# Kernel optimization log

Measured on AMD Instinct MI355X. Metric: run time of the kernel, lower is better.

## Reference

```python
import jax, jax.numpy as jnp
import numpy as np

NUM_HEADS = 8
GS = 7  # group_size (window) side

def _relative_position_index():
    # static index table, matches the torch meshgrid('ij') construction
    coords = np.stack(np.meshgrid(np.arange(GS), np.arange(GS), indexing='ij'))  # (2,GS,GS)
    cf = coords.reshape(2, -1)                                 # (2, 49)
    rel = cf[:, :, None] - cf[:, None, :]                      # (2, 49, 49)
    rel = rel.transpose(1, 2, 0).copy()                        # (49, 49, 2)
    rel[..., 0] += GS - 1
    rel[..., 1] += GS - 1
    rel[..., 0] *= 2 * GS - 1
    return rel.sum(-1)                                         # (49, 49) in [0, 169)

REL_INDEX = jnp.asarray(_relative_position_index())

def setup_inputs() -> dict:
    key = jax.random.key(0)
    ks = jax.random.split(key, 5)
    B, N, C = 2048, 49, 256
    HID = 64
    return {
        'q': jax.random.normal(ks[0], (B, N, C), dtype=jnp.float32),
        'k': jax.random.normal(ks[1], (B, N, C), dtype=jnp.float32),
        'v': jax.random.normal(ks[2], (B, N, C), dtype=jnp.float32),
        'W1': jax.random.normal(ks[3], (2, HID), dtype=jnp.float32) * 0.1,
        'b1': jnp.zeros((HID,), dtype=jnp.float32),
        'W2': jax.random.normal(ks[4], (HID, NUM_HEADS), dtype=jnp.float32) * 0.1,
        'b2': jnp.zeros((NUM_HEADS,), dtype=jnp.float32),
        'H': 56,
        'W': 56,
    }

def _bias_table(W1, b1, W2, b2):
    # biases: (2*GS-1)^2 relative offsets, dpb_pos modeled as 2-layer MLP 2->HID->heads
    r = jnp.arange(1 - GS, GS, dtype=jnp.float32)
    bh, bw = jnp.meshgrid(r, r, indexing='ij')
    biases = jnp.stack([bh.ravel(), bw.ravel()], axis=1)       # (169, 2)
    pos = jax.nn.relu(biases @ W1 + b1) @ W2 + b2              # (169, heads)
    return pos[REL_INDEX].transpose(2, 0, 1)                   # (heads, 49, 49)

def reference(q, k, v, W1, b1, W2, b2, H, W):
    B, N, C = q.shape
    h = NUM_HEADS
    d = C // h
    scale = d ** -0.5
    qh = q.reshape(B, N, h, d)
    kh = k.reshape(B, N, h, d)
    vh = v.reshape(B, N, h, d)
    attn = jnp.einsum('bihd,bjhd->bhij', qh, kh) * scale       # (B,h,N,N)
    bias = _bias_table(W1, b1, W2, b2)                         # (h,49,49)
    if H == 7 and W == 7:
        attn = attn.at[:, :, 0:GS * GS, 0:GS * GS].add(bias[None])
    else:
        attn = attn + bias[None]
    attn = jax.nn.softmax(attn, axis=-1)
    out = jnp.einsum('bhij,bjhd->bihd', attn, vh).reshape(B, N, C)
    return out
```

## Files before the change

### kernel.cpp

```cpp
#include <hip/hip_runtime.h>

typedef __attribute__((ext_vector_type(4))) _Float16 f16x4;
typedef __attribute__((ext_vector_type(8))) _Float16 f16x8;
typedef __attribute__((ext_vector_type(4))) float f32x4;

#define NWIN 49
#define NH 8
#define CCH 256

__device__ __forceinline__ uint cvt2_u32(float a, float b) {
    auto t = __builtin_amdgcn_cvt_pkrtz(a, b);
    return *(uint*)&t;
}
__device__ __forceinline__ f16x4 mk4(uint a, uint b) {
    union { uint u[2]; f16x4 v; } x;
    x.u[0] = a; x.u[1] = b;
    return x.v;
}
__device__ __forceinline__ f16x8 mk8(uint a, uint b, uint c, uint d) {
    union { uint u[4]; f16x8 v; } x;
    x.u[0] = a; x.u[1] = b; x.u[2] = c; x.u[3] = d;
    return x.v;
}

__global__ void pos_mlp_kernel(const float* __restrict__ W1, const float* __restrict__ b1,
                               const float* __restrict__ W2, const float* __restrict__ b2,
                               float* __restrict__ pos) {
    int idx = blockIdx.x * blockDim.x + threadIdx.x;
    if (idx >= 169) return;
    float bh = (float)(idx / 13) - 6.0f;
    float bw = (float)(idx % 13) - 6.0f;
    float outv[NH];
#pragma unroll
    for (int t = 0; t < NH; ++t) outv[t] = b2[t];
    for (int u = 0; u < 64; ++u) {
        float hv = fmaf(bh, W1[u], fmaf(bw, W1[64 + u], b1[u]));
        hv = fmaxf(hv, 0.0f);
#pragma unroll
        for (int t = 0; t < NH; ++t) outv[t] = fmaf(hv, W2[u * NH + t], outv[t]);
    }
#pragma unroll
    for (int t = 0; t < NH; ++t) pos[idx * NH + t] = outv[t];
}

__global__ void bias_frag_kernel(const float* __restrict__ pos, float* __restrict__ bfrag) {
    int blk = blockIdx.x;
    int it = blk & 3, jt = (blk >> 2) & 3, h = blk >> 4;
    int lane = threadIdx.x;
    int g = lane >> 4, l15 = lane & 15;
    int i = it * 16 + l15;
    float4 v;
    float* vp = (float*)&v;
#pragma unroll
    for (int r = 0; r < 4; ++r) {
        int j = jt * 16 + g * 4 + r;
        float val;
        if (j >= NWIN) val = -1e30f;
        else if (i >= NWIN) val = 0.0f;
        else {
            int rel = (i / 7 - j / 7 + 6) * 13 + (i % 7 - j % 7 + 6);
            val = pos[rel * NH + h] * 1.4426950408889634f;
        }
        vp[r] = val;
    }
    *(float4*)(bfrag + (size_t)blk * 256 + lane * 4) = v;
}

__global__ __launch_bounds__(512, 3) void attn_kernel(
    const float* __restrict__ q, const float* __restrict__ k,
    const float* __restrict__ v, const float* __restrict__ bfrag,
    float* __restrict__ out) {
    const int nper = (int)(gridDim.x >> 3);
    const int b = ((int)blockIdx.x & 7) * nper + ((int)blockIdx.x >> 3);

    const int tid = threadIdx.x;
    const int w = tid >> 6, lane = tid & 63;
    const int h = w;
    const int g = lane >> 4, l15 = lane & 15;
    const size_t base = (size_t)b * (NWIN * CCH) + h * 32;

    float4 kraw[4][2], qraw[4][2];
#pragma unroll
    for (int t = 0; t < 4; ++t) {
        int row = t * 16 + l15;
        int rc = row < NWIN ? row : NWIN - 1;
        const float* kp = k + base + (size_t)rc * CCH + g * 8;
        const float* qp = q + base + (size_t)rc * CCH + g * 8;
        kraw[t][0] = *(const float4*)kp; kraw[t][1] = *(const float4*)(kp + 4);
        qraw[t][0] = *(const float4*)qp; qraw[t][1] = *(const float4*)(qp + 4);
    }
    float vv[4][2][4];
#pragma unroll
    for (int jt = 0; jt < 4; ++jt)
#pragma unroll
        for (int nt = 0; nt < 2; ++nt)
#pragma unroll
            for (int r = 0; r < 4; ++r) {
                int j = jt * 16 + 4 * g + r;
                int jc = j < NWIN ? j : NWIN - 1;
                vv[jt][nt][r] = v[base + (size_t)jc * CCH + nt * 16 + l15];
            }

#pragma unroll
    for (int t = 0; t < 4; ++t)
        asm volatile("" :: "v"(kraw[t][0].x), "v"(kraw[t][1].x),
                           "v"(qraw[t][0].x), "v"(qraw[t][1].x));

    f16x8 ka16[4], qb16[4];
#pragma unroll
    for (int t = 0; t < 4; ++t) {
        float4 a = kraw[t][0], c = kraw[t][1];
        ka16[t] = mk8(cvt2_u32(a.x, a.y), cvt2_u32(a.z, a.w),
                      cvt2_u32(c.x, c.y), cvt2_u32(c.z, c.w));
        float4 d = qraw[t][0], e = qraw[t][1];
        qb16[t] = mk8(cvt2_u32(d.x, d.y), cvt2_u32(d.z, d.w),
                      cvt2_u32(e.x, e.y), cvt2_u32(e.z, e.w));
    }

    f32x4 acc[4][4];
#pragma unroll
    for (int jt = 0; jt < 4; ++jt)
#pragma unroll
        for (int it = 0; it < 4; ++it) {
            f32x4 a = {0.f, 0.f, 0.f, 0.f};
            acc[jt][it] = __builtin_amdgcn_mfma_f32_16x16x32_f16(ka16[jt], qb16[it], a, 0, 0, 0);
        }

    f32x4 bb[4][4];
#pragma unroll
    for (int jt = 0; jt < 4; ++jt)
#pragma unroll
        for (int it = 0; it < 4; ++it)
            bb[jt][it] = *(const f32x4*)(bfrag + (size_t)((h * 4 + jt) * 4 + it) * 256 + lane * 4);

    const float scale2 = 0.17677669529663687f * 1.4426950408889634f;
    f16x4 pfrag[4][4];
#pragma unroll
    for (int it = 0; it < 4; ++it) {
        float p[16];
        float s = 0.0f;
#pragma unroll
        for (int jt = 0; jt < 4; ++jt)
#pragma unroll
            for (int r = 0; r < 4; ++r) {
                float e = __builtin_amdgcn_exp2f(fmaf(acc[jt][it][r], scale2, bb[jt][it][r]));
                p[jt * 4 + r] = e;
                s += e;
            }
        s += __shfl_xor(s, 16);
        s += __shfl_xor(s, 32);
        const float inv = 1.0f / s;
#pragma unroll
        for (int jt = 0; jt < 4; ++jt)
            pfrag[jt][it] = mk4(cvt2_u32(p[jt * 4 + 0] * inv, p[jt * 4 + 1] * inv),
                                cvt2_u32(p[jt * 4 + 2] * inv, p[jt * 4 + 3] * inv));
    }

#pragma unroll
    for (int jt = 0; jt < 4; ++jt)
        asm volatile("" :: "v"(vv[jt][0][0]), "v"(vv[jt][0][3]),
                           "v"(vv[jt][1][0]), "v"(vv[jt][1][3]));
    f16x4 vfrag[4][2];
#pragma unroll
    for (int jt = 0; jt < 4; ++jt)
#pragma unroll
        for (int nt = 0; nt < 2; ++nt)
            vfrag[jt][nt] = mk4(cvt2_u32(vv[jt][nt][0], vv[jt][nt][1]),
                                cvt2_u32(vv[jt][nt][2], vv[jt][nt][3]));

    f32x4 oacc[4][2];
#pragma unroll
    for (int mt = 0; mt < 4; ++mt)
#pragma unroll
        for (int nt = 0; nt < 2; ++nt) oacc[mt][nt] = (f32x4){0.f, 0.f, 0.f, 0.f};
#pragma unroll
    for (int jt = 0; jt < 4; ++jt)
#pragma unroll
        for (int mt = 0; mt < 4; ++mt)
#pragma unroll
            for (int nt = 0; nt < 2; ++nt)
                oacc[mt][nt] = __builtin_amdgcn_mfma_f32_16x16x16f16(pfrag[jt][mt], vfrag[jt][nt],
                                                                     oacc[mt][nt], 0, 0, 0);

#pragma unroll
    for (int mt = 0; mt < 4; ++mt)
#pragma unroll
        for (int r = 0; r < 4; ++r) {
            int i = mt * 16 + g * 4 + r;
            if (i < NWIN) {
                float* op = out + base + (size_t)i * CCH + l15;
                op[0]  = oacc[mt][0][r];
                op[16] = oacc[mt][1][r];
            }
        }
}

extern "C" void kernel_launch(void* const* d_in, const int* in_sizes, int n_in,
                              void* d_out, int out_size, void* d_ws, size_t ws_size,
                              hipStream_t stream) {
    const float* q  = (const float*)d_in[0];
    const float* k  = (const float*)d_in[1];
    const float* v  = (const float*)d_in[2];
    const float* W1 = (const float*)d_in[3];
    const float* b1 = (const float*)d_in[4];
    const float* W2 = (const float*)d_in[5];
    const float* b2 = (const float*)d_in[6];

    float* pos   = (float*)d_ws;
    float* bfrag = (float*)((char*)d_ws + 8192);
    float* out   = (float*)d_out;

    const int B = in_sizes[0] / (NWIN * CCH);

    pos_mlp_kernel<<<1, 192, 0, stream>>>(W1, b1, W2, b2, pos);
    bias_frag_kernel<<<128, 64, 0, stream>>>(pos, bfrag);
    attn_kernel<<<B, 512, 0, stream>>>(q, k, v, bfrag, out);
}
```

Baseline: 108.6 us.

## Process two windows per block, fuse bias MLP kernels, store bias in fp16

Each attention block now handles two batch windows. It preloads Q/K for both up front and issues window B's V loads before computing window B, so memory latency overlaps with compute and bias fragments are loaded once per two windows. The two bias setup kernels are merged into one that evaluates the MLP per fragment element and packs the bias as fp16, which removes a launch and halves bias reads. In exchange register pressure rises (launch bounds drop to 2 blocks/SM), the grid is halved, and fp16 bias adds some rounding. The kernel also assumes B is even.

```diff
diff --git a/kernel.cpp b/kernel.cpp
--- a/kernel.cpp
+++ b/kernel.cpp
@@ -22,74 +22,82 @@
     x.u[0] = a; x.u[1] = b; x.u[2] = c; x.u[3] = d;
     return x.v;
 }
-
-__global__ void pos_mlp_kernel(const float* __restrict__ W1, const float* __restrict__ b1,
-                               const float* __restrict__ W2, const float* __restrict__ b2,
-                               float* __restrict__ pos) {
-    int idx = blockIdx.x * blockDim.x + threadIdx.x;
-    if (idx >= 169) return;
-    float bh = (float)(idx / 13) - 6.0f;
-    float bw = (float)(idx % 13) - 6.0f;
-    float outv[NH];
-#pragma unroll
-    for (int t = 0; t < NH; ++t) outv[t] = b2[t];
-    for (int u = 0; u < 64; ++u) {
-        float hv = fmaf(bh, W1[u], fmaf(bw, W1[64 + u], b1[u]));
-        hv = fmaxf(hv, 0.0f);
-#pragma unroll
-        for (int t = 0; t < NH; ++t) outv[t] = fmaf(hv, W2[u * NH + t], outv[t]);
-    }
-#pragma unroll
-    for (int t = 0; t < NH; ++t) pos[idx * NH + t] = outv[t];
-}
-
-__global__ void bias_frag_kernel(const float* __restrict__ pos, float* __restrict__ bfrag) {
+__device__ __forceinline__ float bias_elem(uint2 bb, int r) {
+    union { uint u; _Float16 h[2]; } x;
+    x.u = (r < 2) ? bb.x : bb.y;
+    return (float)x.h[r & 1];
+}
+
+__global__ void bias16_kernel(const float* __restrict__ W1, const float* __restrict__ b1,
+                              const float* __restrict__ W2, const float* __restrict__ b2,
+                              uint* __restrict__ bfrag16) {
     int blk = blockIdx.x;
     int it = blk & 3, jt = (blk >> 2) & 3, h = blk >> 4;
     int lane = threadIdx.x;
     int g = lane >> 4, l15 = lane & 15;
     int i = it * 16 + l15;
-    float4 v;
-    float* vp = (float*)&v;
+    int ic = i < NWIN ? i : NWIN - 1;
+    float dh[4], dw[4], outv[4];
+#pragma unroll
+    for (int r = 0; r < 4; ++r) {
+        int j = jt * 16 + g * 4 + r;
+        int jc = j < NWIN ? j : NWIN - 1;
+        dh[r] = (float)(ic / 7 - jc / 7);
+        dw[r] = (float)(ic % 7 - jc % 7);
+        outv[r] = b2[h];
+    }
+    for (int u = 0; u < 64; ++u) {
+        float w1a = W1[u], w1b = W1[64 + u], bu = b1[u], w2 = W2[u * NH + h];
+#pragma unroll
+        for (int r = 0; r < 4; ++r) {
+            float hv = fmaxf(fmaf(dh[r], w1a, fmaf(dw[r], w1b, bu)), 0.0f);
+            outv[r] = fmaf(hv, w2, outv[r]);
+        }
+    }
+    _Float16 hv16[4];
 #pragma unroll
     for (int r = 0; r < 4; ++r) {
         int j = jt * 16 + g * 4 + r;
         float val;
-        if (j >= NWIN) val = -1e30f;
+        if (j >= NWIN) val = -__builtin_inff();
         else if (i >= NWIN) val = 0.0f;
-        else {
-            int rel = (i / 7 - j / 7 + 6) * 13 + (i % 7 - j % 7 + 6);
-            val = pos[rel * NH + h] * 1.4426950408889634f;
-        }
-        vp[r] = val;
-    }
-    *(float4*)(bfrag + (size_t)blk * 256 + lane * 4) = v;
-}
-
-__global__ __launch_bounds__(512, 3) void attn_kernel(
+        else val = outv[r] * 1.4426950408889634f;
+        hv16[r] = (_Float16)val;
+    }
+    union { _Float16 h[4]; uint2 u; } pk;
+    pk.h[0] = hv16[0]; pk.h[1] = hv16[1]; pk.h[2] = hv16[2]; pk.h[3] = hv16[3];
+    *(uint2*)(bfrag16 + (size_t)blk * 128 + lane * 2) = pk.u;
+}
+
+__global__ __launch_bounds__(512, 2) void attn_kernel(
     const float* __restrict__ q, const float* __restrict__ k,
-    const float* __restrict__ v, const float* __restrict__ bfrag,
+    const float* __restrict__ v, const uint* __restrict__ bfrag16,
     float* __restrict__ out) {
     const int nper = (int)(gridDim.x >> 3);
-    const int b = ((int)blockIdx.x & 7) * nper + ((int)blockIdx.x >> 3);
+    const int bw = ((int)blockIdx.x & 7) * nper + ((int)blockIdx.x >> 3);
 
     const int tid = threadIdx.x;
     const int w = tid >> 6, lane = tid & 63;
     const int h = w;
     const int g = lane >> 4, l15 = lane & 15;
-    const size_t base = (size_t)b * (NWIN * CCH) + h * 32;
-
-    float4 kraw[4][2], qraw[4][2];
+    const size_t baseA = (size_t)(2 * bw) * (NWIN * CCH) + h * 32;
+    const size_t baseB = baseA + (size_t)NWIN * CCH;
+
+    float4 kA[4][2], qA[4][2], kB[4][2], qB[4][2];
 #pragma unroll
     for (int t = 0; t < 4; ++t) {
         int row = t * 16 + l15;
         int rc = row < NWIN ? row : NWIN - 1;
-        const float* kp = k + base + (size_t)rc * CCH + g * 8;
-        const float* qp = q + base + (size_t)rc * CCH + g * 8;
-        kraw[t][0] = *(const float4*)kp; kraw[t][1] = *(const float4*)(kp + 4);
-        qraw[t][0] = *(const float4*)qp; qraw[t][1] = *(const float4*)(qp + 4);
-    }
-    float vv[4][2][4];
+        const float* kpA = k + baseA + (size_t)rc * CCH + g * 8;
+        const float* qpA = q + baseA + (size_t)rc * CCH + g * 8;
+        const float* kpB = k + baseB + (size_t)rc * CCH + g * 8;
+        const float* qpB = q + baseB + (size_t)rc * CCH + g * 8;
+        kA[t][0] = *(const float4*)kpA; kA[t][1] = *(const float4*)(kpA + 4);
+        qA[t][0] = *(const float4*)qpA; qA[t][1] = *(const float4*)(qpA + 4);
+        kB[t][0] = *(const float4*)kpB; kB[t][1] = *(const float4*)(kpB + 4);
+        qB[t][0] = *(const float4*)qpB; qB[t][1] = *(const float4*)(qpB + 4);
+    }
+    float vA[4][2][4];
 #pragma unroll
     for (int jt = 0; jt < 4; ++jt)
 #pragma unroll
@@ -98,25 +106,27 @@
             for (int r = 0; r < 4; ++r) {
                 int j = jt * 16 + 4 * g + r;
                 int jc = j < NWIN ? j : NWIN - 1;
-                vv[jt][nt][r] = v[base + (size_t)jc * CCH + nt * 16 + l15];
-            }
+                vA[jt][nt][r] = v[baseA + (size_t)jc * CCH + nt * 16 + l15];
+            }
+    uint2 bb16[4][4];
+#pragma unroll
+    for (int jt = 0; jt < 4; ++jt)
+#pragma unroll
+        for (int it = 0; it < 4; ++it)
+            bb16[jt][it] = *(const uint2*)(bfrag16 + (size_t)((h * 4 + jt) * 4 + it) * 128 + lane * 2);
+
+    const float scale2 = 0.17677669529663687f * 1.4426950408889634f;
 
 #pragma unroll
     for (int t = 0; t < 4; ++t)
-        asm volatile("" :: "v"(kraw[t][0].x), "v"(kraw[t][1].x),
-                           "v"(qraw[t][0].x), "v"(qraw[t][1].x));
-
+        asm volatile("" :: "v"(kA[t][0].x), "v"(kA[t][1].x), "v"(qA[t][0].x), "v"(qA[t][1].x));
     f16x8 ka16[4], qb16[4];
 #pragma unroll
     for (int t = 0; t < 4; ++t) {
-        float4 a = kraw[t][0], c = kraw[t][1];
-        ka16[t] = mk8(cvt2_u32(a.x, a.y), cvt2_u32(a.z, a.w),
-                      cvt2_u32(c.x, c.y), cvt2_u32(c.z, c.w));
-        float4 d = qraw[t][0], e = qraw[t][1];
-        qb16[t] = mk8(cvt2_u32(d.x, d.y), cvt2_u32(d.z, d.w),
-                      cvt2_u32(e.x, e.y), cvt2_u32(e.z, e.w));
-    }
-
+        float4 a = kA[t][0], c = kA[t][1], d = qA[t][0], e = qA[t][1];
+        ka16[t] = mk8(cvt2_u32(a.x, a.y), cvt2_u32(a.z, a.w), cvt2_u32(c.x, c.y), cvt2_u32(c.z, c.w));
+        qb16[t] = mk8(cvt2_u32(d.x, d.y), cvt2_u32(d.z, d.w), cvt2_u32(e.x, e.y), cvt2_u32(e.z, e.w));
+    }
     f32x4 acc[4][4];
 #pragma unroll
     for (int jt = 0; jt < 4; ++jt)
@@ -125,16 +135,11 @@
             f32x4 a = {0.f, 0.f, 0.f, 0.f};
             acc[jt][it] = __builtin_amdgcn_mfma_f32_16x16x32_f16(ka16[jt], qb16[it], a, 0, 0, 0);
         }
-
-    f32x4 bb[4][4];
-#pragma unroll
-    for (int jt = 0; jt < 4; ++jt)
-#pragma unroll
-        for (int it = 0; it < 4; ++it)
-            bb[jt][it] = *(const f32x4*)(bfrag + (size_t)((h * 4 + jt) * 4 + it) * 256 + lane * 4);
-
-    const float scale2 = 0.17677669529663687f * 1.4426950408889634f;
-    f16x4 pfrag[4][4];
+#pragma unroll
+    for (int jt = 0; jt < 4; ++jt)
+        asm volatile("" :: "v"(bb16[jt][0].x), "v"(bb16[jt][1].x), "v"(bb16[jt][2].x), "v"(bb16[jt][3].x));
+
+    f16x4 pf[4][4];
 #pragma unroll
     for (int it = 0; it < 4; ++it) {
         float p[16];
@@ -143,7 +148,7 @@
         for (int jt = 0; jt < 4; ++jt)
 #pragma unroll
             for (int r = 0; r < 4; ++r) {
-                float e = __builtin_amdgcn_exp2f(fmaf(acc[jt][it][r], scale2, bb[jt][it][r]));
+                float e = __builtin_amdgcn_exp2f(fmaf(acc[jt][it][r], scale2, bias_elem(bb16[jt][it], r)));
                 p[jt * 4 + r] = e;
                 s += e;
             }
@@ -152,22 +157,18 @@
         const float inv = 1.0f / s;
 #pragma unroll
         for (int jt = 0; jt < 4; ++jt)
-            pfrag[jt][it] = mk4(cvt2_u32(p[jt * 4 + 0] * inv, p[jt * 4 + 1] * inv),
-                                cvt2_u32(p[jt * 4 + 2] * inv, p[jt * 4 + 3] * inv));
-    }
-
-#pragma unroll
-    for (int jt = 0; jt < 4; ++jt)
-        asm volatile("" :: "v"(vv[jt][0][0]), "v"(vv[jt][0][3]),
-                           "v"(vv[jt][1][0]), "v"(vv[jt][1][3]));
-    f16x4 vfrag[4][2];
-#pragma unroll
-    for (int jt = 0; jt < 4; ++jt)
-#pragma unroll
-        for (int nt = 0; nt < 2; ++nt)
-            vfrag[jt][nt] = mk4(cvt2_u32(vv[jt][nt][0], vv[jt][nt][1]),
-                                cvt2_u32(vv[jt][nt][2], vv[jt][nt][3]));
-
+            pf[jt][it] = mk4(cvt2_u32(p[jt * 4 + 0] * inv, p[jt * 4 + 1] * inv),
+                             cvt2_u32(p[jt * 4 + 2] * inv, p[jt * 4 + 3] * inv));
+    }
+#pragma unroll
+    for (int jt = 0; jt < 4; ++jt)
+        asm volatile("" :: "v"(vA[jt][0][0]), "v"(vA[jt][0][3]), "v"(vA[jt][1][0]), "v"(vA[jt][1][3]));
+    f16x4 vf[4][2];
+#pragma unroll
+    for (int jt = 0; jt < 4; ++jt)
+#pragma unroll
+        for (int nt = 0; nt < 2; ++nt)
+            vf[jt][nt] = mk4(cvt2_u32(vA[jt][nt][0], vA[jt][nt][1]), cvt2_u32(vA[jt][nt][2], vA[jt][nt][3]));
     f32x4 oacc[4][2];
 #pragma unroll
     for (int mt = 0; mt < 4; ++mt)
@@ -179,16 +180,93 @@
         for (int mt = 0; mt < 4; ++mt)
 #pragma unroll
             for (int nt = 0; nt < 2; ++nt)
-                oacc[mt][nt] = __builtin_amdgcn_mfma_f32_16x16x16f16(pfrag[jt][mt], vfrag[jt][nt],
-                                                                     oacc[mt][nt], 0, 0, 0);
-
+                oacc[mt][nt] = __builtin_amdgcn_mfma_f32_16x16x16f16(pf[jt][mt], vf[jt][nt], oacc[mt][nt], 0, 0, 0);
 #pragma unroll
     for (int mt = 0; mt < 4; ++mt)
 #pragma unroll
         for (int r = 0; r < 4; ++r) {
             int i = mt * 16 + g * 4 + r;
             if (i < NWIN) {
-                float* op = out + base + (size_t)i * CCH + l15;
+                float* op = out + baseA + (size_t)i * CCH + l15;
+                op[0]  = oacc[mt][0][r];
+                op[16] = oacc[mt][1][r];
+            }
+        }
+
+    float vB[4][2][4];
+#pragma unroll
+    for (int jt = 0; jt < 4; ++jt)
+#pragma unroll
+        for (int nt = 0; nt < 2; ++nt)
+#pragma unroll
+            for (int r = 0; r < 4; ++r) {
+                int j = jt * 16 + 4 * g + r;
+                int jc = j < NWIN ? j : NWIN - 1;
+                vB[jt][nt][r] = v[baseB + (size_t)jc * CCH + nt * 16 + l15];
+            }
+
+#pragma unroll
+    for (int t = 0; t < 4; ++t)
+        asm volatile("" :: "v"(kB[t][0].x), "v"(kB[t][1].x), "v"(qB[t][0].x), "v"(qB[t][1].x));
+#pragma unroll
+    for (int t = 0; t < 4; ++t) {
+        float4 a = kB[t][0], c = kB[t][1], d = qB[t][0], e = qB[t][1];
+        ka16[t] = mk8(cvt2_u32(a.x, a.y), cvt2_u32(a.z, a.w), cvt2_u32(c.x, c.y), cvt2_u32(c.z, c.w));
+        qb16[t] = mk8(cvt2_u32(d.x, d.y), cvt2_u32(d.z, d.w), cvt2_u32(e.x, e.y), cvt2_u32(e.z, e.w));
+    }
+#pragma unroll
+    for (int jt = 0; jt < 4; ++jt)
+#pragma unroll
+        for (int it = 0; it < 4; ++it) {
+            f32x4 a = {0.f, 0.f, 0.f, 0.f};
+            acc[jt][it] = __builtin_amdgcn_mfma_f32_16x16x32_f16(ka16[jt], qb16[it], a, 0, 0, 0);
+        }
+#pragma unroll
+    for (int it = 0; it < 4; ++it) {
+        float p[16];
+        float s = 0.0f;
+#pragma unroll
+        for (int jt = 0; jt < 4; ++jt)
+#pragma unroll
+            for (int r = 0; r < 4; ++r) {
+                float e = __builtin_amdgcn_exp2f(fmaf(acc[jt][it][r], scale2, bias_elem(bb16[jt][it], r)));
+                p[jt * 4 + r] = e;
+                s += e;
+            }
+        s += __shfl_xor(s, 16);
+        s += __shfl_xor(s, 32);
+        const float inv = 1.0f / s;
+#pragma unroll
+        for (int jt = 0; jt < 4; ++jt)
+            pf[jt][it] = mk4(cvt2_u32(p[jt * 4 + 0] * inv, p[jt * 4 + 1] * inv),
+                             cvt2_u32(p[jt * 4 + 2] * inv, p[jt * 4 + 3] * inv));
+    }
+#pragma unroll
+    for (int jt = 0; jt < 4; ++jt)
+        asm volatile("" :: "v"(vB[jt][0][0]), "v"(vB[jt][0][3]), "v"(vB[jt][1][0]), "v"(vB[jt][1][3]));
+#pragma unroll
+    for (int jt = 0; jt < 4; ++jt)
+#pragma unroll
+        for (int nt = 0; nt < 2; ++nt)
+            vf[jt][nt] = mk4(cvt2_u32(vB[jt][nt][0], vB[jt][nt][1]), cvt2_u32(vB[jt][nt][2], vB[jt][nt][3]));
+#pragma unroll
+    for (int mt = 0; mt < 4; ++mt)
+#pragma unroll
+        for (int nt = 0; nt < 2; ++nt) oacc[mt][nt] = (f32x4){0.f, 0.f, 0.f, 0.f};
+#pragma unroll
+    for (int jt = 0; jt < 4; ++jt)
+#pragma unroll
+        for (int mt = 0; mt < 4; ++mt)
+#pragma unroll
+            for (int nt = 0; nt < 2; ++nt)
+                oacc[mt][nt] = __builtin_amdgcn_mfma_f32_16x16x16f16(pf[jt][mt], vf[jt][nt], oacc[mt][nt], 0, 0, 0);
+#pragma unroll
+    for (int mt = 0; mt < 4; ++mt)
+#pragma unroll
+        for (int r = 0; r < 4; ++r) {
+            int i = mt * 16 + g * 4 + r;
+            if (i < NWIN) {
+                float* op = out + baseB + (size_t)i * CCH + l15;
                 op[0]  = oacc[mt][0][r];
                 op[16] = oacc[mt][1][r];
             }
@@ -206,13 +284,11 @@
     const float* W2 = (const float*)d_in[5];
     const float* b2 = (const float*)d_in[6];
 
-    float* pos   = (float*)d_ws;
-    float* bfrag = (float*)((char*)d_ws + 8192);
-    float* out   = (float*)d_out;
+    uint* bfrag16 = (uint*)d_ws;
+    float* out    = (float*)d_out;
 
     const int B = in_sizes[0] / (NWIN * CCH);
 
-    pos_mlp_kernel<<<1, 192, 0, stream>>>(W1, b1, W2, b2, pos);
-    bias_frag_kernel<<<128, 64, 0, stream>>>(pos, bfrag);
-    attn_kernel<<<B, 512, 0, stream>>>(q, k, v, bfrag, out);
-}
+    bias16_kernel<<<128, 64, 0, stream>>>(W1, b1, W2, b2, bfrag16);
+    attn_kernel<<<B / 2, 512, 0, stream>>>(q, k, v, bfrag16, out);
+}
```

After: 123.2 us. 1.13x slower.

## Stage Q/K/V and output through LDS with coalesced float4 global access

Applied to the files above, without the earlier changes.

Each block now loads the whole 49x256 window of q, k and v with fully coalesced float4 loads. It converts them to fp16 into shared memory, storing V transposed, and then reads MFMA fragments from LDS. The output is gathered in LDS and written back as coalesced float4 rows instead of strided 16-lane scalar stores. This targets inefficient global access, especially the scalar V gathers and scattered stores. In exchange it uses roughly 78KB of LDS per block, which likely caps residency below the raised launch-bounds target, and it adds barriers and bank-conflicting scalar transposed V writes.

```diff
diff --git a/kernel.cpp b/kernel.cpp
--- a/kernel.cpp
+++ b/kernel.cpp
@@ -7,6 +7,10 @@
 #define NWIN 49
 #define NH 8
 #define CCH 256
+#define NF4 3136
+#define QROW 264
+#define VROW 52
+#define OROW 260
 
 __device__ __forceinline__ uint cvt2_u32(float a, float b) {
     auto t = __builtin_amdgcn_cvt_pkrtz(a, b);
@@ -15,11 +19,6 @@
 __device__ __forceinline__ f16x4 mk4(uint a, uint b) {
     union { uint u[2]; f16x4 v; } x;
     x.u[0] = a; x.u[1] = b;
-    return x.v;
-}
-__device__ __forceinline__ f16x8 mk8(uint a, uint b, uint c, uint d) {
-    union { uint u[4]; f16x8 v; } x;
-    x.u[0] = a; x.u[1] = b; x.u[2] = c; x.u[3] = d;
     return x.v;
 }
 
@@ -66,10 +65,16 @@
     *(float4*)(bfrag + (size_t)blk * 256 + lane * 4) = v;
 }
 
-__global__ __launch_bounds__(512, 3) void attn_kernel(
+__global__ __launch_bounds__(512, 4) void attn_kernel(
     const float* __restrict__ q, const float* __restrict__ k,
     const float* __restrict__ v, const float* __restrict__ bfrag,
     float* __restrict__ out) {
+    __shared__ __align__(16) ushort pool[39184];
+    ushort* qh = pool;
+    ushort* kh = pool + 12936;
+    ushort* vT = pool + 25872;
+    float* ldsOut = (float*)pool;
+
     const int nper = (int)(gridDim.x >> 3);
     const int b = ((int)blockIdx.x & 7) * nper + ((int)blockIdx.x >> 3);
 
@@ -77,45 +82,57 @@
     const int w = tid >> 6, lane = tid & 63;
     const int h = w;
     const int g = lane >> 4, l15 = lane & 15;
-    const size_t base = (size_t)b * (NWIN * CCH) + h * 32;
-
-    float4 kraw[4][2], qraw[4][2];
+    const size_t wbase = (size_t)b * (NWIN * CCH);
+
+#pragma unroll
+    for (int it = 0; it < 7; ++it) {
+        int s = it * 512 + tid;
+        if (s < NF4) {
+            int row = s >> 6;
+            int col = (s & 63) * 4;
+            float4 q4 = *(const float4*)(q + wbase + (size_t)s * 4);
+            float4 k4 = *(const float4*)(k + wbase + (size_t)s * 4);
+            float4 v4 = *(const float4*)(v + wbase + (size_t)s * 4);
+            uint2 qw; qw.x = cvt2_u32(q4.x, q4.y); qw.y = cvt2_u32(q4.z, q4.w);
+            uint2 kw; kw.x = cvt2_u32(k4.x, k4.y); kw.y = cvt2_u32(k4.z, k4.w);
+            uint v01 = cvt2_u32(v4.x, v4.y), v23 = cvt2_u32(v4.z, v4.w);
+            *(uint2*)&qh[row * QROW + col] = qw;
+            *(uint2*)&kh[row * QROW + col] = kw;
+            vT[(col + 0) * VROW + row] = (ushort)(v01 & 0xffffu);
+            vT[(col + 1) * VROW + row] = (ushort)(v01 >> 16);
+            vT[(col + 2) * VROW + row] = (ushort)(v23 & 0xffffu);
+            vT[(col + 3) * VROW + row] = (ushort)(v23 >> 16);
+        }
+    }
+    __syncthreads();
+
+    f16x8 ka16[4], qb16[4];
 #pragma unroll
     for (int t = 0; t < 4; ++t) {
         int row = t * 16 + l15;
         int rc = row < NWIN ? row : NWIN - 1;
-        const float* kp = k + base + (size_t)rc * CCH + g * 8;
-        const float* qp = q + base + (size_t)rc * CCH + g * 8;
-        kraw[t][0] = *(const float4*)kp; kraw[t][1] = *(const float4*)(kp + 4);
-        qraw[t][0] = *(const float4*)qp; qraw[t][1] = *(const float4*)(qp + 4);
-    }
-    float vv[4][2][4];
-#pragma unroll
-    for (int jt = 0; jt < 4; ++jt)
+        ka16[t] = *(const f16x8*)&kh[rc * QROW + h * 32 + g * 8];
+        qb16[t] = *(const f16x8*)&qh[rc * QROW + h * 32 + g * 8];
+    }
+    f16x4 vf[4][2];
+#pragma unroll
+    for (int jt = 0; jt < 3; ++jt)
 #pragma unroll
         for (int nt = 0; nt < 2; ++nt)
-#pragma unroll
-            for (int r = 0; r < 4; ++r) {
-                int j = jt * 16 + 4 * g + r;
-                int jc = j < NWIN ? j : NWIN - 1;
-                vv[jt][nt][r] = v[base + (size_t)jc * CCH + nt * 16 + l15];
-            }
-
-#pragma unroll
-    for (int t = 0; t < 4; ++t)
-        asm volatile("" :: "v"(kraw[t][0].x), "v"(kraw[t][1].x),
-                           "v"(qraw[t][0].x), "v"(qraw[t][1].x));
-
-    f16x8 ka16[4], qb16[4];
-#pragma unroll
-    for (int t = 0; t < 4; ++t) {
-        float4 a = kraw[t][0], c = kraw[t][1];
-        ka16[t] = mk8(cvt2_u32(a.x, a.y), cvt2_u32(a.z, a.w),
-                      cvt2_u32(c.x, c.y), cvt2_u32(c.z, c.w));
-        float4 d = qraw[t][0], e = qraw[t][1];
-        qb16[t] = mk8(cvt2_u32(d.x, d.y), cvt2_u32(d.z, d.w),
-                      cvt2_u32(e.x, e.y), cvt2_u32(e.z, e.w));
-    }
+            vf[jt][nt] = *(const f16x4*)&vT[(h * 32 + nt * 16 + l15) * VROW + jt * 16 + 4 * g];
+#pragma unroll
+    for (int nt = 0; nt < 2; ++nt) {
+        int colbase = (h * 32 + nt * 16 + l15) * VROW;
+        union { ushort u[4]; f16x4 v; } x;
+#pragma unroll
+        for (int r = 0; r < 4; ++r) {
+            int j = 48 + 4 * g + r;
+            int jc = j < NWIN ? j : NWIN - 1;
+            x.u[r] = vT[colbase + jc];
+        }
+        vf[3][nt] = x.v;
+    }
+    __syncthreads();
 
     f32x4 acc[4][4];
 #pragma unroll
@@ -126,60 +143,43 @@
             acc[jt][it] = __builtin_amdgcn_mfma_f32_16x16x32_f16(ka16[jt], qb16[it], a, 0, 0, 0);
         }
 
-    f32x4 bb[4][4];
-#pragma unroll
-    for (int jt = 0; jt < 4; ++jt)
-#pragma unroll
-        for (int it = 0; it < 4; ++it)
-            bb[jt][it] = *(const f32x4*)(bfrag + (size_t)((h * 4 + jt) * 4 + it) * 256 + lane * 4);
-
     const float scale2 = 0.17677669529663687f * 1.4426950408889634f;
-    f16x4 pfrag[4][4];
+    f16x4 pf[4][4];
 #pragma unroll
     for (int it = 0; it < 4; ++it) {
         float p[16];
         float s = 0.0f;
 #pragma unroll
-        for (int jt = 0; jt < 4; ++jt)
+        for (int jt = 0; jt < 4; ++jt) {
+            f32x4 bb = *(const f32x4*)(bfrag + (size_t)((h * 4 + jt) * 4 + it) * 256 + lane * 4);
 #pragma unroll
             for (int r = 0; r < 4; ++r) {
-                float e = __builtin_amdgcn_exp2f(fmaf(acc[jt][it][r], scale2, bb[jt][it][r]));
+                float e = __builtin_amdgcn_exp2f(fmaf(acc[jt][it][r], scale2, bb[r]));
                 p[jt * 4 + r] = e;
                 s += e;
             }
+        }
         s += __shfl_xor(s, 16);
         s += __shfl_xor(s, 32);
         const float inv = 1.0f / s;
 #pragma unroll
         for (int jt = 0; jt < 4; ++jt)
-            pfrag[jt][it] = mk4(cvt2_u32(p[jt * 4 + 0] * inv, p[jt * 4 + 1] * inv),
-                                cvt2_u32(p[jt * 4 + 2] * inv, p[jt * 4 + 3] * inv));
-    }
-
+            pf[jt][it] = mk4(cvt2_u32(p[jt * 4 + 0] * inv, p[jt * 4 + 1] * inv),
+                             cvt2_u32(p[jt * 4 + 2] * inv, p[jt * 4 + 3] * inv));
+    }
+
+    f32x4 oacc[4][2];
+#pragma unroll
+    for (int mt = 0; mt < 4; ++mt)
+#pragma unroll
+        for (int nt = 0; nt < 2; ++nt) oacc[mt][nt] = (f32x4){0.f, 0.f, 0.f, 0.f};
 #pragma unroll
     for (int jt = 0; jt < 4; ++jt)
-        asm volatile("" :: "v"(vv[jt][0][0]), "v"(vv[jt][0][3]),
-                           "v"(vv[jt][1][0]), "v"(vv[jt][1][3]));
-    f16x4 vfrag[4][2];
-#pragma unroll
-    for (int jt = 0; jt < 4; ++jt)
-#pragma unroll
-        for (int nt = 0; nt < 2; ++nt)
-            vfrag[jt][nt] = mk4(cvt2_u32(vv[jt][nt][0], vv[jt][nt][1]),
-                                cvt2_u32(vv[jt][nt][2], vv[jt][nt][3]));
-
-    f32x4 oacc[4][2];
-#pragma unroll
-    for (int mt = 0; mt < 4; ++mt)
-#pragma unroll
-        for (int nt = 0; nt < 2; ++nt) oacc[mt][nt] = (f32x4){0.f, 0.f, 0.f, 0.f};
-#pragma unroll
-    for (int jt = 0; jt < 4; ++jt)
 #pragma unroll
         for (int mt = 0; mt < 4; ++mt)
 #pragma unroll
             for (int nt = 0; nt < 2; ++nt)
-                oacc[mt][nt] = __builtin_amdgcn_mfma_f32_16x16x16f16(pfrag[jt][mt], vfrag[jt][nt],
+                oacc[mt][nt] = __builtin_amdgcn_mfma_f32_16x16x16f16(pf[jt][mt], vf[jt][nt],
                                                                      oacc[mt][nt], 0, 0, 0);
 
 #pragma unroll
@@ -187,12 +187,20 @@
 #pragma unroll
         for (int r = 0; r < 4; ++r) {
             int i = mt * 16 + g * 4 + r;
-            if (i < NWIN) {
-                float* op = out + base + (size_t)i * CCH + l15;
-                op[0]  = oacc[mt][0][r];
-                op[16] = oacc[mt][1][r];
-            }
-        }
+            ldsOut[i * OROW + h * 32 + l15]      = oacc[mt][0][r];
+            ldsOut[i * OROW + h * 32 + 16 + l15] = oacc[mt][1][r];
+        }
+    __syncthreads();
+
+#pragma unroll
+    for (int it = 0; it < 7; ++it) {
+        int s = it * 512 + tid;
+        if (s < NF4) {
+            int row = s >> 6;
+            int col = (s & 63) * 4;
+            *(float4*)(out + wbase + (size_t)s * 4) = *(const float4*)&ldsOut[row * OROW + col];
+        }
+    }
 }
 
 extern "C" void kernel_launch(void* const* d_in, const int* in_sizes, int n_in,
```

Measured after the change: 111.5 us. 2.7% more time.
